# Kernel tuning notes

Hardware: AMD Instinct MI355X
Metric: run time of the kernel (lower is better)

The kernel has to match this reference:

```python
import jax, jax.numpy as jnp
import numpy as np

D_MODEL = 512
N_HEAD = 8
D_K = D_MODEL // N_HEAD
B, S = 4, 2048


def setup_inputs() -> dict:
    key = jax.random.key(0)
    ks = jax.random.split(key, 13)
    scale = 1.0 / np.sqrt(D_MODEL)
    inp = {
        "query": jax.random.normal(ks[0], (B, S, D_MODEL), jnp.float32),
        "key": jax.random.normal(ks[1], (B, S, D_MODEL), jnp.float32),
        "value": jax.random.normal(ks[2], (B, S, D_MODEL), jnp.float32),
        "mask": jax.random.randint(ks[3], (B, S, S), 0, 2).astype(bool),
        "Wq": jax.random.normal(ks[4], (D_MODEL, D_MODEL), jnp.float32) * scale,
        "bq": jax.random.normal(ks[5], (D_MODEL,), jnp.float32) * scale,
        "Wk": jax.random.normal(ks[6], (D_MODEL, D_MODEL), jnp.float32) * scale,
        "bk": jax.random.normal(ks[7], (D_MODEL,), jnp.float32) * scale,
        "Wv": jax.random.normal(ks[8], (D_MODEL, D_MODEL), jnp.float32) * scale,
        "bv": jax.random.normal(ks[9], (D_MODEL,), jnp.float32) * scale,
        "Wo": jax.random.normal(ks[10], (D_MODEL, D_MODEL), jnp.float32) * scale,
        "bo": jax.random.normal(ks[11], (D_MODEL,), jnp.float32) * scale,
    }
    return inp


def reference(query, key, value, mask, Wq, bq, Wk, bk, Wv, bv, Wo, bo):
    b = query.shape[0]
    # QKV projections -> [b, h, s, d_k]
    q = (query @ Wq.T + bq).reshape(b, -1, N_HEAD, D_K).transpose(0, 2, 1, 3)
    k = (key @ Wk.T + bk).reshape(b, -1, N_HEAD, D_K).transpose(0, 2, 1, 3)
    v = (value @ Wv.T + bv).reshape(b, -1, N_HEAD, D_K).transpose(0, 2, 1, 3)
    # scaled dot-product scores [b, h, sq, sk]
    scores = jnp.einsum("bhqd,bhkd->bhqk", q, k) / jnp.sqrt(jnp.float32(D_K))
    # masked_fill(mask, -1e4): mask broadcast over heads
    scores = jnp.where(mask[:, None, :, :], jnp.float32(-10000.0), scores)
    attn = jax.nn.softmax(scores, axis=-1)
    x = jnp.einsum("bhqk,bhkd->bhqd", attn, v)
    x = x.transpose(0, 2, 1, 3).reshape(b, -1, N_HEAD * D_K)
    return x @ Wo.T + bo
```

## Files before the change

kernel.cpp:

```cpp
#include <hip/hip_runtime.h>
#include <hip/hip_bf16.h>

#define DMODEL 512
#define NHEAD  8
#define DKH    64
#define SEQ    2048
#define NB     4
#define LOG2E  1.44269504088896f

typedef float f32x4 __attribute__((ext_vector_type(4)));
typedef float f32x16 __attribute__((ext_vector_type(16)));
typedef short bf16x8 __attribute__((ext_vector_type(8)));

__device__ __forceinline__ unsigned short f2bf(float x) {
    unsigned int u = __float_as_uint(x);
    u += 0x7fffu + ((u >> 16) & 1u);
    return (unsigned short)(u >> 16);
}

__device__ __forceinline__ void gload16(const void* g, void* l) {
    __builtin_amdgcn_global_load_lds(
        (const __attribute__((address_space(1))) unsigned int*)g,
        (__attribute__((address_space(3))) unsigned int*)l, 16, 0, 0);
}

__device__ __forceinline__ unsigned int cvtpk(float lo, float hi) {
    unsigned int r;
    asm("v_cvt_pk_bf16_f32 %0, %1, %2" : "=v"(r) : "v"(lo), "v"(hi));
    return r;
}

#define CVT_BLOCKS  6656
#define PACK_BLOCKS 1024
struct PrepArgs {
    const float* src[7]; unsigned short* dst[7];
    const unsigned char* mask; unsigned long long* bits;
};

__global__ __launch_bounds__(256) void prep(PrepArgs a)
{
    const int bx = blockIdx.x;
    if (bx < CVT_BLOCKS) {
        int seg, base;
        if (bx < 6144) { seg = bx >> 11; base = bx & 2047; }
        else           { const int w = bx - 6144; seg = 3 + (w >> 7); base = w & 127; }
        const int i = (base * 256 + threadIdx.x) * 8;
        const float* s = a.src[seg];
        const float4 v0 = *reinterpret_cast<const float4*>(s + i);
        const float4 v1 = *reinterpret_cast<const float4*>(s + i + 4);
        ushort4 h0, h1;
        h0.x = f2bf(v0.x); h0.y = f2bf(v0.y); h0.z = f2bf(v0.z); h0.w = f2bf(v0.w);
        h1.x = f2bf(v1.x); h1.y = f2bf(v1.y); h1.z = f2bf(v1.z); h1.w = f2bf(v1.w);
        *reinterpret_cast<ushort4*>(a.dst[seg] + i)     = h0;
        *reinterpret_cast<ushort4*>(a.dst[seg] + i + 4) = h1;
    } else {
        __shared__ int anyb;
        if (threadIdx.x == 0) anyb = 0;
        __syncthreads();
        const uint4 dv = *reinterpret_cast<const uint4*>(a.mask + threadIdx.x * 16);
        if ((dv.x | dv.y | dv.z | dv.w) & 0xFFFFFF00u) atomicOr(&anyb, 1);
        __syncthreads();
        const int bytemode = anyb;

        const int w = (bx - CVT_BLOCKS) * 256 + threadIdx.x;
        const int b = w >> 16, kt = (w >> 11) & 31, row = w & 2047;
        const size_t eoff = ((size_t)(b * SEQ + row)) * SEQ + kt * 64;
        unsigned long long word = 0;
        if (bytemode) {
            const unsigned char* mp = a.mask + eoff;
            #pragma unroll
            for (int c = 0; c < 4; ++c) {
                const uint4 v = *reinterpret_cast<const uint4*>(mp + c * 16);
                const unsigned int n0 = (v.x | (v.x >> 7) | (v.x >> 14) | (v.x >> 21)) & 0xFu;
                const unsigned int n1 = (v.y | (v.y >> 7) | (v.y >> 14) | (v.y >> 21)) & 0xFu;
                const unsigned int n2 = (v.z | (v.z >> 7) | (v.z >> 14) | (v.z >> 21)) & 0xFu;
                const unsigned int n3 = (v.w | (v.w >> 7) | (v.w >> 14) | (v.w >> 21)) & 0xFu;
                const unsigned int ch = n0 | (n1 << 4) | (n2 << 8) | (n3 << 12);
                word |= (unsigned long long)ch << (16 * c);
            }
        } else {
            const unsigned int* mp = (const unsigned int*)a.mask + eoff;
            #pragma unroll
            for (int c = 0; c < 16; ++c) {
                const uint4 v = *reinterpret_cast<const uint4*>(mp + c * 4);
                const unsigned int nb = (v.x | (v.y << 1) | (v.z << 2) | (v.w << 3)) & 0xFu;
                word |= (unsigned long long)nb << (4 * c);
            }
        }
        a.bits[w] = word;
    }
}

struct GemmSet {
    const unsigned short* A; const unsigned short* W; const float* bias;
    unsigned short* outb; float* outf; float scale; int mode;
};
struct Gemm3 { GemmSet s[3]; };

template<int BM>
__global__ __launch_bounds__(256) void gemm_bf16(Gemm3 G)
{
    constexpr int NJ = (BM == 128) ? 4 : 2;
    __shared__ unsigned short As[BM * 64];
    __shared__ unsigned short Bs[128 * 64];

    const GemmSet gs = G.s[blockIdx.z];
    const int tid = threadIdx.x, lane = tid & 63, wv = tid >> 6;
    const int g = lane >> 4, lr = lane & 15;
    const int bm = blockIdx.x * BM, bn = blockIdx.y * 128;
    const int wm = (BM == 128) ? (wv & 1) * 64 : 0;
    const int wn = (BM == 128) ? (wv >> 1) * 64 : wv * 32;
    const int srow = lane >> 3;
    const int scol = 8 * ((lane & 7) ^ srow);

    f32x4 acc[4][NJ] = {};

    for (int kt = 0; kt < DMODEL; kt += 64) {
        __syncthreads();
        #pragma unroll
        for (int i = 0; i < BM / 32; ++i) {
            const int ch = i * 4 + wv;
            const int row = ch * 8 + srow;
            gload16(&gs.A[(size_t)(bm + row) * DMODEL + kt + scol], &As[ch * 512 + lane * 8]);
        }
        #pragma unroll
        for (int i = 0; i < 4; ++i) {
            const int ch = i * 4 + wv;
            const int row = ch * 8 + srow;
            gload16(&gs.W[(size_t)(bn + row) * DMODEL + kt + scol], &Bs[ch * 512 + lane * 8]);
        }
        __syncthreads();

        #pragma unroll
        for (int kk = 0; kk < 2; ++kk) {
            bf16x8 af[4], bfr[NJ];
            #pragma unroll
            for (int x = 0; x < 4; ++x) {
                const int ra = wm + x * 16 + lr;
                af[x] = *reinterpret_cast<const bf16x8*>(
                    (const char*)As + ((ra * 128 + kk * 64 + g * 16) ^ ((ra & 7) << 4)));
            }
            #pragma unroll
            for (int y = 0; y < NJ; ++y) {
                const int rb = wn + y * 16 + lr;
                bfr[y] = *reinterpret_cast<const bf16x8*>(
                    (const char*)Bs + ((rb * 128 + kk * 64 + g * 16) ^ ((rb & 7) << 4)));
            }
            __builtin_amdgcn_s_setprio(1);
            #pragma unroll
            for (int mi = 0; mi < 4; ++mi)
                #pragma unroll
                for (int nj = 0; nj < NJ; ++nj)
                    acc[mi][nj] = __builtin_amdgcn_mfma_f32_16x16x32_bf16(af[mi], bfr[nj], acc[mi][nj], 0, 0, 0);
            __builtin_amdgcn_s_setprio(0);
        }
    }

    const int mode = gs.mode;
    #pragma unroll
    for (int mi = 0; mi < 4; ++mi) {
        #pragma unroll
        for (int nj = 0; nj < NJ; ++nj) {
            const int col  = bn + wn + nj * 16 + lr;
            const int row0 = bm + wm + mi * 16 + g * 4;
            const float bv = gs.bias[col];
            if (mode == 2) {
                const int bb = row0 >> 11, ss = row0 & (SEQ - 1);
                const int hh = col >> 6,  dd = col & 63;
                ushort4 pk;
                pk.x = f2bf(acc[mi][nj][0] + bv);
                pk.y = f2bf(acc[mi][nj][1] + bv);
                pk.z = f2bf(acc[mi][nj][2] + bv);
                pk.w = f2bf(acc[mi][nj][3] + bv);
                *reinterpret_cast<ushort4*>(&gs.outb[((size_t)((bb * NHEAD + hh) * DKH + dd)) * SEQ + ss]) = pk;
            } else if (mode == 3) {
                #pragma unroll
                for (int r = 0; r < 4; ++r)
                    gs.outf[(size_t)(row0 + r) * DMODEL + col] = acc[mi][nj][r] + bv;
            } else {
                #pragma unroll
                for (int r = 0; r < 4; ++r)
                    gs.outb[(size_t)(row0 + r) * DMODEL + col] = f2bf((acc[mi][nj][r] + bv) * gs.scale);
            }
        }
    }
}

__global__ __launch_bounds__(256) void attn_fwd(
    const unsigned short* __restrict__ Q,
    const unsigned short* __restrict__ K,
    const unsigned short* __restrict__ Vt,
    const unsigned long long* __restrict__ bits,
    unsigned short* __restrict__ X)
{
    __shared__ unsigned short Ks[2][64 * 64];
    __shared__ unsigned short Vs[2][64 * 64];

    const int tid = threadIdx.x, lane = tid & 63, wv = tid >> 6;
    const int lr32 = lane & 31, hi = lane >> 5;
    const int bid = blockIdx.x;
    const int wg  = (bid & 7) * 64 + (bid >> 3);
    const int qb = wg & 15, h = (wg >> 4) & 7, b = wg >> 7;
    const int q0 = qb * 128, qw = q0 + wv * 32;

    const unsigned short* Kbh = K  + (size_t)b * SEQ * DMODEL + h * DKH;
    const unsigned short* Vbh = Vt + (size_t)(b * NHEAD + h) * DKH * SEQ;
    const unsigned long long* bitsb = bits + (size_t)b * 32 * SEQ + qw + lr32;

    bf16x8 qf[4];
    #pragma unroll
    for (int kd = 0; kd < 4; ++kd)
        qf[kd] = *reinterpret_cast<const bf16x8*>(
            &Q[(size_t)(b * SEQ + qw + lr32) * DMODEL + h * DKH + kd * 16 + hi * 8]);

    const int srow = lane >> 3;
    const int scol = 8 * ((lane & 7) ^ srow);

    auto stage = [&](int buf, int kt) {
        #pragma unroll
        for (int i = 0; i < 2; ++i) {
            const int ch  = i * 4 + wv;
            const int row = ch * 8 + srow;
            gload16(&Kbh[(size_t)(kt + row) * DMODEL + scol], &Ks[buf][ch * 512 + lane * 8]);
            gload16(&Vbh[(size_t)row * SEQ + kt + scol],      &Vs[buf][ch * 512 + lane * 8]);
        }
    };

    union { unsigned int u[4]; bf16x8 v; } onesu;
    onesu.u[0] = onesu.u[1] = onesu.u[2] = onesu.u[3] = 0x3F803F80u;
    const bf16x8 ones = onesu.v;

    f32x16 o0 = {}, o1 = {}, o_sum = {};

    stage(0, 0);
    __syncthreads();

    for (int t = 0; t < 32; ++t) {
        const int cur = t & 1;
        if (t < 31) stage(cur ^ 1, (t + 1) * 64);

        const unsigned long long mw  = bitsb[(size_t)t * SEQ];
        const unsigned long long msh = mw >> (4 * hi);
        const unsigned int mlo = (unsigned int)msh;
        const unsigned int mhi = (unsigned int)(msh >> 32);

        f32x16 s0 = {}, s1 = {};
        __builtin_amdgcn_s_setprio(1);
        #pragma unroll
        for (int kd = 0; kd < 4; ++kd) {
            const int cb = kd * 32 + hi * 16;
            const int r0 = lr32, r1 = 32 + lr32;
            const bf16x8 kf0 = *reinterpret_cast<const bf16x8*>(
                (const char*)Ks[cur] + ((r0 * 128 + cb) ^ ((r0 & 7) << 4)));
            const bf16x8 kf1 = *reinterpret_cast<const bf16x8*>(
                (const char*)Ks[cur] + ((r1 * 128 + cb) ^ ((r1 & 7) << 4)));
            s0 = __builtin_amdgcn_mfma_f32_32x32x16_bf16(kf0, qf[kd], s0, 0, 0, 0);
            s1 = __builtin_amdgcn_mfma_f32_32x32x16_bf16(kf1, qf[kd], s1, 0, 0, 0);
        }
        __builtin_amdgcn_s_setprio(0);

        unsigned int pk[8][2];
        #pragma unroll
        for (int kj = 0; kj < 2; ++kj) {
            const unsigned int msel = kj ? mhi : mlo;
            #pragma unroll
            for (int o2 = 0; o2 < 4; ++o2) {
                float p[4];
                #pragma unroll
                for (int r = 0; r < 4; ++r) {
                    const int bitp = o2 * 8 + r;
                    const float mf = (float)(msel & (1u << bitp));
                    const float coef = -1024.f / (float)(1u << bitp);
                    const float sv = kj ? s1[o2 * 4 + r] : s0[o2 * 4 + r];
                    p[r] = exp2f(__builtin_fmaf(mf, coef, sv));
                }
                pk[kj * 4 + o2][0] = cvtpk(p[0], p[1]);
                pk[kj * 4 + o2][1] = cvtpk(p[2], p[3]);
            }
        }

        #pragma unroll
        for (int kk = 0; kk < 4; ++kk) {
            unsigned int a0 = pk[2 * kk][0], b0 = pk[2 * kk + 1][0];
            unsigned int a1 = pk[2 * kk][1], b1 = pk[2 * kk + 1][1];
            asm("v_permlane32_swap_b32 %0, %1" : "+v"(a0), "+v"(b0));
            asm("v_permlane32_swap_b32 %0, %1" : "+v"(a1), "+v"(b1));
            union { unsigned int u[4]; bf16x8 v; } fr;
            fr.u[0] = a0; fr.u[1] = a1; fr.u[2] = b0; fr.u[3] = b1;
            const int cb = kk * 32 + hi * 16;
            const int r0 = lr32, r1 = 32 + lr32;
            const bf16x8 vf0 = *reinterpret_cast<const bf16x8*>(
                (const char*)Vs[cur] + ((r0 * 128 + cb) ^ ((r0 & 7) << 4)));
            const bf16x8 vf1 = *reinterpret_cast<const bf16x8*>(
                (const char*)Vs[cur] + ((r1 * 128 + cb) ^ ((r1 & 7) << 4)));
            __builtin_amdgcn_s_setprio(1);
            o0    = __builtin_amdgcn_mfma_f32_32x32x16_bf16(fr.v, vf0, o0, 0, 0, 0);
            o1    = __builtin_amdgcn_mfma_f32_32x32x16_bf16(fr.v, vf1, o1, 0, 0, 0);
            o_sum = __builtin_amdgcn_mfma_f32_32x32x16_bf16(fr.v, ones, o_sum, 0, 0, 0);
            __builtin_amdgcn_s_setprio(0);
        }

        __syncthreads();
    }

    #pragma unroll
    for (int r = 0; r < 16; ++r) {
        const int qr = (r & 3) + 8 * (r >> 2) + 4 * hi;
        const float rv = 1.f / o_sum[r];
        const size_t rowoff = (size_t)(b * SEQ + qw + qr) * DMODEL + h * DKH + lr32;
        X[rowoff]      = f2bf(o0[r] * rv);
        X[rowoff + 32] = f2bf(o1[r] * rv);
    }
}

extern "C" void kernel_launch(void* const* d_in, const int* in_sizes, int n_in,
                              void* d_out, int out_size, void* d_ws, size_t ws_size,
                              hipStream_t stream)
{
    const float* query = (const float*)d_in[0];
    const float* key   = (const float*)d_in[1];
    const float* value = (const float*)d_in[2];
    const unsigned char* mask = (const unsigned char*)d_in[3];
    const float* Wq = (const float*)d_in[4];
    const float* bq = (const float*)d_in[5];
    const float* Wk = (const float*)d_in[6];
    const float* bk = (const float*)d_in[7];
    const float* Wv = (const float*)d_in[8];
    const float* bv = (const float*)d_in[9];
    const float* Wo = (const float*)d_in[10];
    const float* bo = (const float*)d_in[11];

    const size_t E = (size_t)(NB * SEQ) * DMODEL;
    const size_t WE = (size_t)DMODEL * DMODEL;
    unsigned short* Qc  = (unsigned short*)d_ws;
    unsigned short* Kc  = Qc + E;
    unsigned short* Vc  = Kc + E;
    unsigned short* Qp  = Vc + E;
    unsigned short* Kp  = Qp + E;
    unsigned short* Vtp = Kp + E;
    unsigned short* Wqb = Vtp + E;
    unsigned short* Wkb = Wqb + WE;
    unsigned short* Wvb = Wkb + WE;
    unsigned short* Wob = Wvb + WE;
    unsigned long long* bits = (unsigned long long*)(Wob + WE);
    unsigned short* Xp = Qc;

    PrepArgs pa;
    pa.src[0] = query; pa.src[1] = key; pa.src[2] = value;
    pa.src[3] = Wq; pa.src[4] = Wk; pa.src[5] = Wv; pa.src[6] = Wo;
    pa.dst[0] = Qc; pa.dst[1] = Kc; pa.dst[2] = Vc;
    pa.dst[3] = Wqb; pa.dst[4] = Wkb; pa.dst[5] = Wvb; pa.dst[6] = Wob;
    pa.mask = mask; pa.bits = bits;
    prep<<<dim3(CVT_BLOCKS + PACK_BLOCKS), 256, 0, stream>>>(pa);

    Gemm3 gq;
    gq.s[0] = { Qc, Wqb, bq, Qp,  nullptr, 0.125f * LOG2E, 0 };
    gq.s[1] = { Kc, Wkb, bk, Kp,  nullptr, 1.0f,   0 };
    gq.s[2] = { Vc, Wvb, bv, Vtp, nullptr, 1.0f,   2 };
    gemm_bf16<128><<<dim3(64, 4, 3), 256, 0, stream>>>(gq);

    attn_fwd<<<dim3(512), 256, 0, stream>>>(Qp, Kp, Vtp, bits, Xp);

    Gemm3 go;
    go.s[0] = { Xp, Wob, bo, nullptr, (float*)d_out, 1.0f, 3 };
    go.s[1] = go.s[0]; go.s[2] = go.s[0];
    gemm_bf16<64><<<dim3(128, 4, 1), 256, 0, stream>>>(go);
}
```

Baseline: 147.7 us.

## Split attention KV loop across two wave groups with LDS reduction

Doubles the attention block to 512 threads, with the second group of four waves processing alternate 64-key halves of each 128-key chunk. This halves the serial loop length per wave and raises waves per CU to hide latency. At the end, partial numerators and denominators are combined through LDS. In exchange the block uses twice the shared memory and needs an extra reduction and barrier. Softmax without max-subtraction makes the split additive, so it stays correct.

```diff
diff --git a/kernel.cpp b/kernel.cpp
--- a/kernel.cpp
+++ b/kernel.cpp
@@ -186,22 +186,24 @@
     }
 }
 
-__global__ __launch_bounds__(256) void attn_fwd(
+__global__ __launch_bounds__(512, 4) void attn_fwd(
     const unsigned short* __restrict__ Q,
     const unsigned short* __restrict__ K,
     const unsigned short* __restrict__ Vt,
     const unsigned long long* __restrict__ bits,
     unsigned short* __restrict__ X)
 {
-    __shared__ unsigned short Ks[2][64 * 64];
-    __shared__ unsigned short Vs[2][64 * 64];
+    __shared__ unsigned short Ks[2][2][64 * 64];
+    __shared__ unsigned short Vs[2][2][64 * 64];
 
     const int tid = threadIdx.x, lane = tid & 63, wv = tid >> 6;
+    const int wq = wv & 3;
+    const int hv = wv >> 2;
     const int lr32 = lane & 31, hi = lane >> 5;
     const int bid = blockIdx.x;
     const int wg  = (bid & 7) * 64 + (bid >> 3);
     const int qb = wg & 15, h = (wg >> 4) & 7, b = wg >> 7;
-    const int q0 = qb * 128, qw = q0 + wv * 32;
+    const int q0 = qb * 128, qw = q0 + wq * 32;
 
     const unsigned short* Kbh = K  + (size_t)b * SEQ * DMODEL + h * DKH;
     const unsigned short* Vbh = Vt + (size_t)(b * NHEAD + h) * DKH * SEQ;
@@ -216,13 +218,16 @@
     const int srow = lane >> 3;
     const int scol = 8 * ((lane & 7) ^ srow);
 
-    auto stage = [&](int buf, int kt) {
+    auto stage = [&](int buf, int c) {
         #pragma unroll
         for (int i = 0; i < 2; ++i) {
-            const int ch  = i * 4 + wv;
-            const int row = ch * 8 + srow;
-            gload16(&Kbh[(size_t)(kt + row) * DMODEL + scol], &Ks[buf][ch * 512 + lane * 8]);
-            gload16(&Vbh[(size_t)row * SEQ + kt + scol],      &Vs[buf][ch * 512 + lane * 8]);
+            const int ch   = i * 8 + wv;
+            const int half = ch >> 3;
+            const int chh  = ch & 7;
+            const int row  = chh * 8 + srow;
+            const int kt   = c * 128 + half * 64;
+            gload16(&Kbh[(size_t)(kt + row) * DMODEL + scol], &Ks[buf][half][chh * 512 + lane * 8]);
+            gload16(&Vbh[(size_t)row * SEQ + kt + scol],      &Vs[buf][half][chh * 512 + lane * 8]);
         }
     };
 
@@ -235,14 +240,11 @@
     stage(0, 0);
     __syncthreads();
 
-    for (int t = 0; t < 32; ++t) {
+    for (int t = 0; t < 16; ++t) {
         const int cur = t & 1;
-        if (t < 31) stage(cur ^ 1, (t + 1) * 64);
-
-        const unsigned long long mw  = bitsb[(size_t)t * SEQ];
-        const unsigned long long msh = mw >> (4 * hi);
-        const unsigned int mlo = (unsigned int)msh;
-        const unsigned int mhi = (unsigned int)(msh >> 32);
+        if (t < 15) stage(cur ^ 1, t + 1);
+
+        const unsigned long long mw = bitsb[(size_t)(2 * t + hv) * SEQ];
 
         f32x16 s0 = {}, s1 = {};
         __builtin_amdgcn_s_setprio(1);
@@ -251,14 +253,17 @@
             const int cb = kd * 32 + hi * 16;
             const int r0 = lr32, r1 = 32 + lr32;
             const bf16x8 kf0 = *reinterpret_cast<const bf16x8*>(
-                (const char*)Ks[cur] + ((r0 * 128 + cb) ^ ((r0 & 7) << 4)));
+                (const char*)Ks[cur][hv] + ((r0 * 128 + cb) ^ ((r0 & 7) << 4)));
             const bf16x8 kf1 = *reinterpret_cast<const bf16x8*>(
-                (const char*)Ks[cur] + ((r1 * 128 + cb) ^ ((r1 & 7) << 4)));
+                (const char*)Ks[cur][hv] + ((r1 * 128 + cb) ^ ((r1 & 7) << 4)));
             s0 = __builtin_amdgcn_mfma_f32_32x32x16_bf16(kf0, qf[kd], s0, 0, 0, 0);
             s1 = __builtin_amdgcn_mfma_f32_32x32x16_bf16(kf1, qf[kd], s1, 0, 0, 0);
         }
         __builtin_amdgcn_s_setprio(0);
 
+        const unsigned long long msh = mw >> (4 * hi);
+        const unsigned int mlo = (unsigned int)msh;
+        const unsigned int mhi = (unsigned int)(msh >> 32);
         unsigned int pk[8][2];
         #pragma unroll
         for (int kj = 0; kj < 2; ++kj) {
@@ -288,11 +293,11 @@
             union { unsigned int u[4]; bf16x8 v; } fr;
             fr.u[0] = a0; fr.u[1] = a1; fr.u[2] = b0; fr.u[3] = b1;
             const int cb = kk * 32 + hi * 16;
-            const int r0 = lr32, r1 = 32 + lr32;
+            const int d0 = lr32, d1 = 32 + lr32;
             const bf16x8 vf0 = *reinterpret_cast<const bf16x8*>(
-                (const char*)Vs[cur] + ((r0 * 128 + cb) ^ ((r0 & 7) << 4)));
+                (const char*)Vs[cur][hv] + ((d0 * 128 + cb) ^ ((d0 & 7) << 4)));
             const bf16x8 vf1 = *reinterpret_cast<const bf16x8*>(
-                (const char*)Vs[cur] + ((r1 * 128 + cb) ^ ((r1 & 7) << 4)));
+                (const char*)Vs[cur][hv] + ((d1 * 128 + cb) ^ ((d1 & 7) << 4)));
             __builtin_amdgcn_s_setprio(1);
             o0    = __builtin_amdgcn_mfma_f32_32x32x16_bf16(fr.v, vf0, o0, 0, 0, 0);
             o1    = __builtin_amdgcn_mfma_f32_32x32x16_bf16(fr.v, vf1, o1, 0, 0, 0);
@@ -303,13 +308,33 @@
         __syncthreads();
     }
 
-    #pragma unroll
-    for (int r = 0; r < 16; ++r) {
-        const int qr = (r & 3) + 8 * (r >> 2) + 4 * hi;
-        const float rv = 1.f / o_sum[r];
-        const size_t rowoff = (size_t)(b * SEQ + qw + qr) * DMODEL + h * DKH + lr32;
-        X[rowoff]      = f2bf(o0[r] * rv);
-        X[rowoff + 32] = f2bf(o1[r] * rv);
+    float* cK = (float*)&Ks[0][0][0];
+    float* cV = (float*)&Vs[0][0][0];
+    if (hv == 1) {
+        const int base32 = (wq * 64 + lane) * 32;
+        const int base16 = (wq * 64 + lane) * 16;
+        #pragma unroll
+        for (int r = 0; r < 16; ++r) {
+            cK[base32 + r]      = o0[r];
+            cK[base32 + 16 + r] = o1[r];
+            cV[base16 + r]      = o_sum[r];
+        }
+    }
+    __syncthreads();
+    if (hv == 0) {
+        const int base32 = (wq * 64 + lane) * 32;
+        const int base16 = (wq * 64 + lane) * 16;
+        #pragma unroll
+        for (int r = 0; r < 16; ++r) {
+            const int qr = (r & 3) + 8 * (r >> 2) + 4 * hi;
+            const float num0 = o0[r] + cK[base32 + r];
+            const float num1 = o1[r] + cK[base32 + 16 + r];
+            const float den  = o_sum[r] + cV[base16 + r];
+            const float rv = 1.f / den;
+            const size_t rowoff = (size_t)(b * SEQ + qw + qr) * DMODEL + h * DKH + lr32;
+            X[rowoff]      = f2bf(num0 * rv);
+            X[rowoff + 32] = f2bf(num1 * rv);
+        }
     }
 }
 
@@ -359,7 +384,7 @@
     gq.s[2] = { Vc, Wvb, bv, Vtp, nullptr, 1.0f,   2 };
     gemm_bf16<128><<<dim3(64, 4, 3), 256, 0, stream>>>(gq);
 
-    attn_fwd<<<dim3(512), 256, 0, stream>>>(Qp, Kp, Vtp, bits, Xp);
+    attn_fwd<<<dim3(512), 512, 0, stream>>>(Qp, Kp, Vtp, bits, Xp);
 
     Gemm3 go;
     go.s[0] = { Xp, Wob, bo, nullptr, (float*)d_out, 1.0f, 3 };
```

New measurement: 146.3 us. About the same (-0.9%).
